# Kernel optimization log

Hardware: AMD Instinct MI355X
Metric: run time of the kernel (lower is better)

The kernel has to match this reference:

```python
import jax, jax.numpy as jnp
import numpy as np

N = 500_000   # total nodes across the batch of session graphs
B = 8192      # number of graphs
D = 128       # input_dim == output_dim (fc_out is None)
H = 128       # hidden_dim


def setup_inputs() -> dict:
    key = jax.random.key(0)
    ks = jax.random.split(key, 7)
    x_invar = jax.random.normal(ks[0], (N, D), jnp.float32)
    x_var = jax.random.normal(ks[1], (N, D), jnp.float32)
    s = 1.0 / np.sqrt(D)
    Wu = jax.random.normal(ks[2], (H, D), jnp.float32) * s
    bu = jnp.zeros((H,), jnp.float32)
    Wv = jax.random.normal(ks[3], (H, D), jnp.float32) * s
    We = jax.random.normal(ks[4], (1, H), jnp.float32) * (1.0 / np.sqrt(H))
    # sorted segment ids; guarantee every graph has >= 1 node
    seg_ids = jnp.sort(jnp.concatenate([
        jnp.arange(B, dtype=jnp.int32),
        jax.random.randint(ks[5], (N - B,), 0, B, dtype=jnp.int32),
    ]))
    # last node index of each graph = cumsum(counts) - 1
    counts = jax.ops.segment_sum(jnp.ones((N,), jnp.int32), seg_ids, num_segments=B)
    last_nodes = (jnp.cumsum(counts) - 1).astype(jnp.int32)
    return dict(x_invar=x_invar, x_var=x_var, Wu=Wu, bu=bu, Wv=Wv, We=We,
                seg_ids=seg_ids, last_nodes=last_nodes, num_graphs=B)


def _segment_softmax(e, seg, num_segments):
    # e: [M]; numerically stable per-segment softmax
    m = jax.ops.segment_max(e, seg, num_segments=num_segments)
    ex = jnp.exp(e - m[seg])
    den = jax.ops.segment_sum(ex, seg, num_segments=num_segments)
    return ex / den[seg]


def reference(x_invar, x_var, Wu, bu, Wv, We, seg_ids, last_nodes, num_graphs):
    # hybrid granularity, order=1: per-graph [invar; var] node rows.
    # Segment softmax/sum are permutation-invariant within a segment, so we
    # concatenate globally and double the segment ids.
    feats = jnp.concatenate([x_invar, x_var], axis=0)          # [2N, D]
    seg2 = jnp.concatenate([seg_ids, seg_ids], axis=0)         # [2N]
    feat_u = feats @ Wu.T + bu                                 # [2N, H]
    v_invar = (x_invar[last_nodes] @ Wv.T)[seg2]               # [2N, H]
    v_var = (x_var[last_nodes] @ Wv.T)[seg2]                   # [2N, H]
    e_invar = (jax.nn.sigmoid(feat_u + v_invar) @ We.T)[:, 0]  # [2N]
    e_var = (jax.nn.sigmoid(feat_u + v_var) @ We.T)[:, 0]      # [2N]
    a_invar = _segment_softmax(e_invar, seg2, num_graphs)[:, None]
    a_var = _segment_softmax(e_var, seg2, num_graphs)[:, None]
    rst_invar = jax.ops.segment_sum(feats * a_invar, seg2, num_segments=num_graphs)  # [B, D]
    rst_var = jax.ops.segment_sum(feats * a_var, seg2, num_segments=num_graphs)      # [B, D]
    return rst_invar[:, None, :], rst_var[:, None, :]          # [B, 1, D] each (order=1)
```

## Files before the change

kernel.cpp:

```cpp
#include <hip/hip_runtime.h>
#include <stdint.h>

typedef short short8 __attribute__((ext_vector_type(8)));
typedef float f32x4 __attribute__((ext_vector_type(4)));

#define D 128
#define LOG2E 1.44269504088896340736f

__device__ __forceinline__ unsigned short f2bf(float f) {
    union { float f; unsigned u; } v; v.f = f;
    unsigned u = v.u;
    unsigned r = (u + 0x7FFFu + ((u >> 16) & 1u)) >> 16;
    return (unsigned short)r;
}

__device__ __forceinline__ unsigned packbf(float x, float y) {
    unsigned ux = __float_as_uint(x) + 0x8000u;
    unsigned uy = __float_as_uint(y) + 0x8000u;
    return __builtin_amdgcn_perm(uy, ux, 0x07060302u);
}

template <int C>
__device__ __forceinline__ float dpp_add(float x) {
    int y = __builtin_amdgcn_update_dpp(0, __float_as_int(x), C, 0xF, 0xF, true);
    return x + __int_as_float(y);
}
__device__ __forceinline__ float red16(float x) {
    x = dpp_add<0xB1>(x);
    x = dpp_add<0x4E>(x);
    x = dpp_add<0x141>(x);
    x = dpp_add<0x140>(x);
    return x;
}

__global__ __launch_bounds__(256) void pack_wu(const float* __restrict__ Wu,
                                               short8* __restrict__ frag) {
    int tid = blockIdx.x * 256 + threadIdx.x;
    int nt = tid >> 8, kk = (tid >> 6) & 3, l = tid & 63;
    int col = nt * 16 + (l & 15);
    int kb  = kk * 32 + ((l >> 4) * 8);
    short8 o;
#pragma unroll
    for (int j = 0; j < 8; ++j) o[j] = (short)f2bf(Wu[col * D + kb + j] * LOG2E);
    frag[tid] = o;
}

__global__ __launch_bounds__(256) void gate_k(const float* __restrict__ xI,
                                              const float* __restrict__ xV,
                                              const float* __restrict__ Wv,
                                              const float* __restrict__ bu,
                                              const int* __restrict__ lastn,
                                              float* __restrict__ cIb,
                                              float* __restrict__ cVb, int B) {
    __shared__ __align__(16) float xs[4][2][D];
    int t = threadIdx.x, h = t & 127, st = t >> 7;
    float bias = bu[h];
    const float4* wv4 = (const float4*)(Wv + (size_t)h * D);
    const float* src = st ? xV : xI;
    float* dst = st ? cVb : cIb;
    int g0 = blockIdx.x * 16;
    for (int p = 0; p < 4; ++p) {
        int gb = g0 + p * 4;
#pragma unroll
        for (int j = 0; j < 4; ++j) {
            int gg = gb + j; if (gg >= B) gg = B - 1;
            xs[j][st][h] = src[(size_t)lastn[gg] * D + h];
        }
        __syncthreads();
        const float4* x0 = (const float4*)xs[0][st];
        const float4* x1 = (const float4*)xs[1][st];
        const float4* x2 = (const float4*)xs[2][st];
        const float4* x3 = (const float4*)xs[3][st];
        float a0 = 0.f, a1 = 0.f, a2 = 0.f, a3 = 0.f;
#pragma unroll
        for (int i = 0; i < 32; ++i) {
            float4 w = wv4[i], b;
            b = x0[i]; a0 += w.x*b.x + w.y*b.y + w.z*b.z + w.w*b.w;
            b = x1[i]; a1 += w.x*b.x + w.y*b.y + w.z*b.z + w.w*b.w;
            b = x2[i]; a2 += w.x*b.x + w.y*b.y + w.z*b.z + w.w*b.w;
            b = x3[i]; a3 += w.x*b.x + w.y*b.y + w.z*b.z + w.w*b.w;
        }
        if (gb + 0 < B) dst[(size_t)(gb+0)*D + h] = __builtin_amdgcn_exp2f(-(a0+bias)*LOG2E);
        if (gb + 1 < B) dst[(size_t)(gb+1)*D + h] = __builtin_amdgcn_exp2f(-(a1+bias)*LOG2E);
        if (gb + 2 < B) dst[(size_t)(gb+2)*D + h] = __builtin_amdgcn_exp2f(-(a2+bias)*LOG2E);
        if (gb + 3 < B) dst[(size_t)(gb+3)*D + h] = __builtin_amdgcn_exp2f(-(a3+bias)*LOG2E);
        __syncthreads();
    }
}

__global__ __launch_bounds__(256) void attn_main(
    const float* __restrict__ xI, const float* __restrict__ xV,
    const float* __restrict__ We, const int* __restrict__ lastn,
    const float* __restrict__ cIb, const float* __restrict__ cVb,
    const short8* __restrict__ fragG, float* __restrict__ out, int B) {
    __shared__ short8 bfrag[2048];
    __shared__ __align__(16) float wt[4][16][2];
    __shared__ float cmbA[2][4][D];
    __shared__ float cmbM[2][4], cmbL[2][4];

    int t = threadIdx.x, lane = t & 63, w = t >> 6;
    int g = blockIdx.x;

    {
        const uint4* srcf = (const uint4*)fragG;
        uint4* dst = (uint4*)bfrag;
#pragma unroll
        for (int i = 0; i < 8; ++i) dst[i * 256 + t] = srcf[i * 256 + t];
    }

    int s = (g == 0) ? 0 : (lastn[g - 1] + 1);
    int n = lastn[g] + 1 - s;

    float WeR[8], cIr[8], cVr[8];
#pragma unroll
    for (int nt = 0; nt < 8; ++nt) {
        int col = nt * 16 + (lane & 15);
        WeR[nt] = We[col] * LOG2E;
        cIr[nt] = cIb[(size_t)g * D + col];
        cVr[nt] = cVb[(size_t)g * D + col];
    }
    __syncthreads();

    float mI = -__builtin_inff(), mV = -__builtin_inff();
    float lIs = 0.f, lVs = 0.f;
    float aI0 = 0.f, aI1 = 0.f, aV0 = 0.f, aV1 = 0.f;

    int ch = (n + 15) >> 4;
    int total = 2 * ch;

    for (int c = w; c < total; c += 4) {
        int hf = (c >= ch) ? 1 : 0;
        const float* srcs = (hf ? xV : xI) + ((size_t)s << 7);
        int base = (c - hf * ch) << 4;

        int arow = base + (lane & 15);
        if (arow > n - 1) arow = n - 1;
        const float* rp = srcs + ((size_t)arow << 7) + ((lane >> 4) << 3);
        short8 af[4];
#pragma unroll
        for (int kk = 0; kk < 4; ++kk) {
            float4 f0 = *(const float4*)(rp + kk * 32);
            float4 f1 = *(const float4*)(rp + kk * 32 + 4);
            union { unsigned u[4]; short8 s8; } cv;
            cv.u[0] = packbf(f0.x, f0.y);
            cv.u[1] = packbf(f0.z, f0.w);
            cv.u[2] = packbf(f1.x, f1.y);
            cv.u[3] = packbf(f1.z, f1.w);
            af[kk] = cv.s8;
        }

        float pI[4] = {0.f, 0.f, 0.f, 0.f}, pV[4] = {0.f, 0.f, 0.f, 0.f};
#pragma unroll
        for (int nt = 0; nt < 8; ++nt) {
            f32x4 dacc = {0.f, 0.f, 0.f, 0.f};
#pragma unroll
            for (int kk = 0; kk < 4; ++kk)
                dacc = __builtin_amdgcn_mfma_f32_16x16x32_bf16(
                    af[kk], bfrag[nt * 256 + kk * 64 + lane], dacc, 0, 0, 0);
#pragma unroll
            for (int q = 0; q < 4; ++q) {
                float t2 = __builtin_amdgcn_exp2f(-dacc[q]);
                float dI = fmaf(t2, cIr[nt], 1.f);
                float dV = fmaf(t2, cVr[nt], 1.f);
                float rr = __builtin_amdgcn_rcpf(dI * dV);
                pI[q] = fmaf(WeR[nt], dV * rr, pI[q]);
                pV[q] = fmaf(WeR[nt], dI * rr, pV[q]);
            }
        }
#pragma unroll
        for (int q = 0; q < 4; ++q) { pI[q] = red16(pI[q]); pV[q] = red16(pV[q]); }
        if (base + 16 > n) {
#pragma unroll
            for (int q = 0; q < 4; ++q) {
                int r = ((lane >> 4) << 2) + q;
                if (base + r >= n) { pI[q] = -__builtin_inff(); pV[q] = -__builtin_inff(); }
            }
        }
        float cmI = fmaxf(fmaxf(pI[0], pI[1]), fmaxf(pI[2], pI[3]));
        float cmV = fmaxf(fmaxf(pV[0], pV[1]), fmaxf(pV[2], pV[3]));
        cmI = fmaxf(cmI, __shfl_xor(cmI, 16)); cmI = fmaxf(cmI, __shfl_xor(cmI, 32));
        cmV = fmaxf(cmV, __shfl_xor(cmV, 16)); cmV = fmaxf(cmV, __shfl_xor(cmV, 32));

        float mnI = fmaxf(mI, cmI), mnV = fmaxf(mV, cmV);
        float scI = __builtin_amdgcn_exp2f(mI - mnI);
        float scV = __builtin_amdgcn_exp2f(mV - mnV);
        lIs *= scI; lVs *= scV;
        aI0 *= scI; aI1 *= scI; aV0 *= scV; aV1 *= scV;

        float wIq[4], wVq[4];
#pragma unroll
        for (int q = 0; q < 4; ++q) {
            wIq[q] = __builtin_amdgcn_exp2f(pI[q] - mnI);
            wVq[q] = __builtin_amdgcn_exp2f(pV[q] - mnV);
        }
        float sIq = wIq[0] + wIq[1] + wIq[2] + wIq[3];
        float sVq = wVq[0] + wVq[1] + wVq[2] + wVq[3];
        sIq += __shfl_xor(sIq, 16); sIq += __shfl_xor(sIq, 32);
        sVq += __shfl_xor(sVq, 16); sVq += __shfl_xor(sVq, 32);
        lIs += sIq; lVs += sVq;

        if ((lane & 15) == 0) {
            int gq = lane >> 4;
            float4 w0 = {wIq[0], wVq[0], wIq[1], wVq[1]};
            float4 w1 = {wIq[2], wVq[2], wIq[3], wVq[3]};
            *(float4*)&wt[w][gq * 4 + 0][0] = w0;
            *(float4*)&wt[w][gq * 4 + 2][0] = w1;
        }
        asm volatile("" ::: "memory");

#pragma unroll
        for (int r = 0; r < 16; ++r) {
            int rr = base + r; if (rr > n - 1) rr = n - 1;
            const float* p = srcs + ((size_t)rr << 7);
            float f0 = p[lane], f1 = p[64 + lane];
            float wI = wt[w][r][0], wV = wt[w][r][1];
            aI0 = fmaf(wI, f0, aI0); aI1 = fmaf(wI, f1, aI1);
            aV0 = fmaf(wV, f0, aV0); aV1 = fmaf(wV, f1, aV1);
        }
        mI = mnI; mV = mnV;
    }

    cmbA[0][w][lane] = aI0; cmbA[0][w][lane + 64] = aI1;
    cmbA[1][w][lane] = aV0; cmbA[1][w][lane + 64] = aV1;
    if (lane == 0) {
        cmbM[0][w] = mI; cmbL[0][w] = lIs;
        cmbM[1][w] = mV; cmbL[1][w] = lVs;
    }
    __syncthreads();
    {
        int st = t >> 7, d = t & 127;
        float M = fmaxf(fmaxf(cmbM[st][0], cmbM[st][1]),
                        fmaxf(cmbM[st][2], cmbM[st][3]));
        float Ls = 0.f, A = 0.f;
#pragma unroll
        for (int ww = 0; ww < 4; ++ww) {
            float e = __builtin_amdgcn_exp2f(cmbM[st][ww] - M);
            Ls += cmbL[st][ww] * e;
            A  += cmbA[st][ww][d] * e;
        }
        out[(size_t)st * B * D + (size_t)g * D + d] = A * __builtin_amdgcn_rcpf(Ls);
    }
}

extern "C" void kernel_launch(void* const* d_in, const int* in_sizes, int n_in,
                              void* d_out, int out_size, void* d_ws, size_t ws_size,
                              hipStream_t stream) {
    const float* xI    = (const float*)d_in[0];
    const float* xV    = (const float*)d_in[1];
    const float* Wu    = (const float*)d_in[2];
    const float* bu    = (const float*)d_in[3];
    const float* Wv    = (const float*)d_in[4];
    const float* We    = (const float*)d_in[5];
    const int*   lastn = (const int*)d_in[7];
    const int B = in_sizes[7];

    float*  cIb   = (float*)d_ws;
    float*  cVb   = cIb + (size_t)B * D;
    short8* fragW = (short8*)(cVb + (size_t)B * D);

    pack_wu<<<8, 256, 0, stream>>>(Wu, fragW);
    gate_k<<<(B + 15) / 16, 256, 0, stream>>>(xI, xV, Wv, bu, lastn, cIb, cVb, B);
    attn_main<<<B, 256, 0, stream>>>(xI, xV, We, lastn, cIb, cVb, fragW,
                                     (float*)d_out, B);
}
```

Baseline: 220.8 us.

## Process four graphs per block to amortize weight-fragment LDS staging

Each attention block now handles four consecutive graphs in sequence instead of one, so the 32KB Wu fragment copy into shared memory and the We load are paid once per four graphs. The grid shrinks to B/4 blocks, which lowers parallelism and can hurt load balance across CUs when graph sizes vary. The weighted-sum loop also switches to float2 loads per lane with a matching column layout in the combine buffer. The grid size assumes B is divisible by 4, since any leftover graphs would be skipped.

```diff
diff --git a/kernel.cpp b/kernel.cpp
--- a/kernel.cpp
+++ b/kernel.cpp
@@ -6,6 +6,7 @@
 
 #define D 128
 #define LOG2E 1.44269504088896340736f
+#define GPB 4
 
 __device__ __forceinline__ unsigned short f2bf(float f) {
     union { float f; unsigned u; } v; v.f = f;
@@ -99,7 +100,6 @@
     __shared__ float cmbM[2][4], cmbL[2][4];
 
     int t = threadIdx.x, lane = t & 63, w = t >> 6;
-    int g = blockIdx.x;
 
     {
         const uint4* srcf = (const uint4*)fragG;
@@ -107,138 +107,152 @@
 #pragma unroll
         for (int i = 0; i < 8; ++i) dst[i * 256 + t] = srcf[i * 256 + t];
     }
-
-    int s = (g == 0) ? 0 : (lastn[g - 1] + 1);
-    int n = lastn[g] + 1 - s;
-
-    float WeR[8], cIr[8], cVr[8];
-#pragma unroll
-    for (int nt = 0; nt < 8; ++nt) {
-        int col = nt * 16 + (lane & 15);
-        WeR[nt] = We[col] * LOG2E;
-        cIr[nt] = cIb[(size_t)g * D + col];
-        cVr[nt] = cVb[(size_t)g * D + col];
-    }
+    float WeR[8];
+#pragma unroll
+    for (int nt = 0; nt < 8; ++nt) WeR[nt] = We[nt * 16 + (lane & 15)] * LOG2E;
     __syncthreads();
 
-    float mI = -__builtin_inff(), mV = -__builtin_inff();
-    float lIs = 0.f, lVs = 0.f;
-    float aI0 = 0.f, aI1 = 0.f, aV0 = 0.f, aV1 = 0.f;
-
-    int ch = (n + 15) >> 4;
-    int total = 2 * ch;
-
-    for (int c = w; c < total; c += 4) {
-        int hf = (c >= ch) ? 1 : 0;
-        const float* srcs = (hf ? xV : xI) + ((size_t)s << 7);
-        int base = (c - hf * ch) << 4;
-
-        int arow = base + (lane & 15);
-        if (arow > n - 1) arow = n - 1;
-        const float* rp = srcs + ((size_t)arow << 7) + ((lane >> 4) << 3);
-        short8 af[4];
-#pragma unroll
-        for (int kk = 0; kk < 4; ++kk) {
-            float4 f0 = *(const float4*)(rp + kk * 32);
-            float4 f1 = *(const float4*)(rp + kk * 32 + 4);
-            union { unsigned u[4]; short8 s8; } cv;
-            cv.u[0] = packbf(f0.x, f0.y);
-            cv.u[1] = packbf(f0.z, f0.w);
-            cv.u[2] = packbf(f1.x, f1.y);
-            cv.u[3] = packbf(f1.z, f1.w);
-            af[kk] = cv.s8;
-        }
-
-        float pI[4] = {0.f, 0.f, 0.f, 0.f}, pV[4] = {0.f, 0.f, 0.f, 0.f};
+    int g0 = blockIdx.x * GPB;
+    int sNext = (g0 == 0) ? 0 : (lastn[g0 - 1] + 1);
+
+    for (int gi = 0; gi < GPB; ++gi) {
+        int g = g0 + gi;
+        int s = sNext;
+        int e = lastn[g] + 1;
+        sNext = e;
+        int n = e - s;
+
+        float cIr[8], cVr[8];
 #pragma unroll
         for (int nt = 0; nt < 8; ++nt) {
-            f32x4 dacc = {0.f, 0.f, 0.f, 0.f};
-#pragma unroll
-            for (int kk = 0; kk < 4; ++kk)
-                dacc = __builtin_amdgcn_mfma_f32_16x16x32_bf16(
-                    af[kk], bfrag[nt * 256 + kk * 64 + lane], dacc, 0, 0, 0);
+            int col = nt * 16 + (lane & 15);
+            cIr[nt] = cIb[(size_t)g * D + col];
+            cVr[nt] = cVb[(size_t)g * D + col];
+        }
+
+        float mI = -__builtin_inff(), mV = -__builtin_inff();
+        float lIs = 0.f, lVs = 0.f;
+        float aI0 = 0.f, aI1 = 0.f, aV0 = 0.f, aV1 = 0.f;
+
+        int ch = (n + 15) >> 4;
+        int total = 2 * ch;
+
+        for (int c = w; c < total; c += 4) {
+            int hf = (c >= ch) ? 1 : 0;
+            const float* srcs = (hf ? xV : xI) + ((size_t)s << 7);
+            int base = (c - hf * ch) << 4;
+
+            int arow = base + (lane & 15);
+            if (arow > n - 1) arow = n - 1;
+            const float* rp = srcs + ((size_t)arow << 7) + ((lane >> 4) << 3);
+            short8 af[4];
+#pragma unroll
+            for (int kk = 0; kk < 4; ++kk) {
+                float4 f0 = *(const float4*)(rp + kk * 32);
+                float4 f1 = *(const float4*)(rp + kk * 32 + 4);
+                union { unsigned u[4]; short8 s8; } cv;
+                cv.u[0] = packbf(f0.x, f0.y);
+                cv.u[1] = packbf(f0.z, f0.w);
+                cv.u[2] = packbf(f1.x, f1.y);
+                cv.u[3] = packbf(f1.z, f1.w);
+                af[kk] = cv.s8;
+            }
+
+            float pI[4] = {0.f, 0.f, 0.f, 0.f}, pV[4] = {0.f, 0.f, 0.f, 0.f};
+#pragma unroll
+            for (int nt = 0; nt < 8; ++nt) {
+                f32x4 dacc = {0.f, 0.f, 0.f, 0.f};
+#pragma unroll
+                for (int kk = 0; kk < 4; ++kk)
+                    dacc = __builtin_amdgcn_mfma_f32_16x16x32_bf16(
+                        af[kk], bfrag[nt * 256 + kk * 64 + lane], dacc, 0, 0, 0);
+#pragma unroll
+                for (int q = 0; q < 4; ++q) {
+                    float t2 = __builtin_amdgcn_exp2f(-dacc[q]);
+                    float dI = fmaf(t2, cIr[nt], 1.f);
+                    float dV = fmaf(t2, cVr[nt], 1.f);
+                    float rr = __builtin_amdgcn_rcpf(dI * dV);
+                    pI[q] = fmaf(WeR[nt], dV * rr, pI[q]);
+                    pV[q] = fmaf(WeR[nt], dI * rr, pV[q]);
+                }
+            }
+#pragma unroll
+            for (int q = 0; q < 4; ++q) { pI[q] = red16(pI[q]); pV[q] = red16(pV[q]); }
+            if (base + 16 > n) {
+#pragma unroll
+                for (int q = 0; q < 4; ++q) {
+                    int r = ((lane >> 4) << 2) + q;
+                    if (base + r >= n) { pI[q] = -__builtin_inff(); pV[q] = -__builtin_inff(); }
+                }
+            }
+            float cmI = fmaxf(fmaxf(pI[0], pI[1]), fmaxf(pI[2], pI[3]));
+            float cmV = fmaxf(fmaxf(pV[0], pV[1]), fmaxf(pV[2], pV[3]));
+            cmI = fmaxf(cmI, __shfl_xor(cmI, 16)); cmI = fmaxf(cmI, __shfl_xor(cmI, 32));
+            cmV = fmaxf(cmV, __shfl_xor(cmV, 16)); cmV = fmaxf(cmV, __shfl_xor(cmV, 32));
+
+            float mnI = fmaxf(mI, cmI), mnV = fmaxf(mV, cmV);
+            float scI = __builtin_amdgcn_exp2f(mI - mnI);
+            float scV = __builtin_amdgcn_exp2f(mV - mnV);
+            lIs *= scI; lVs *= scV;
+            aI0 *= scI; aI1 *= scI; aV0 *= scV; aV1 *= scV;
+
+            float wIq[4], wVq[4];
 #pragma unroll
             for (int q = 0; q < 4; ++q) {
-                float t2 = __builtin_amdgcn_exp2f(-dacc[q]);
-                float dI = fmaf(t2, cIr[nt], 1.f);
-                float dV = fmaf(t2, cVr[nt], 1.f);
-                float rr = __builtin_amdgcn_rcpf(dI * dV);
-                pI[q] = fmaf(WeR[nt], dV * rr, pI[q]);
-                pV[q] = fmaf(WeR[nt], dI * rr, pV[q]);
-            }
-        }
-#pragma unroll
-        for (int q = 0; q < 4; ++q) { pI[q] = red16(pI[q]); pV[q] = red16(pV[q]); }
-        if (base + 16 > n) {
-#pragma unroll
-            for (int q = 0; q < 4; ++q) {
-                int r = ((lane >> 4) << 2) + q;
-                if (base + r >= n) { pI[q] = -__builtin_inff(); pV[q] = -__builtin_inff(); }
-            }
-        }
-        float cmI = fmaxf(fmaxf(pI[0], pI[1]), fmaxf(pI[2], pI[3]));
-        float cmV = fmaxf(fmaxf(pV[0], pV[1]), fmaxf(pV[2], pV[3]));
-        cmI = fmaxf(cmI, __shfl_xor(cmI, 16)); cmI = fmaxf(cmI, __shfl_xor(cmI, 32));
-        cmV = fmaxf(cmV, __shfl_xor(cmV, 16)); cmV = fmaxf(cmV, __shfl_xor(cmV, 32));
-
-        float mnI = fmaxf(mI, cmI), mnV = fmaxf(mV, cmV);
-        float scI = __builtin_amdgcn_exp2f(mI - mnI);
-        float scV = __builtin_amdgcn_exp2f(mV - mnV);
-        lIs *= scI; lVs *= scV;
-        aI0 *= scI; aI1 *= scI; aV0 *= scV; aV1 *= scV;
-
-        float wIq[4], wVq[4];
-#pragma unroll
-        for (int q = 0; q < 4; ++q) {
-            wIq[q] = __builtin_amdgcn_exp2f(pI[q] - mnI);
-            wVq[q] = __builtin_amdgcn_exp2f(pV[q] - mnV);
-        }
-        float sIq = wIq[0] + wIq[1] + wIq[2] + wIq[3];
-        float sVq = wVq[0] + wVq[1] + wVq[2] + wVq[3];
-        sIq += __shfl_xor(sIq, 16); sIq += __shfl_xor(sIq, 32);
-        sVq += __shfl_xor(sVq, 16); sVq += __shfl_xor(sVq, 32);
-        lIs += sIq; lVs += sVq;
-
-        if ((lane & 15) == 0) {
-            int gq = lane >> 4;
-            float4 w0 = {wIq[0], wVq[0], wIq[1], wVq[1]};
-            float4 w1 = {wIq[2], wVq[2], wIq[3], wVq[3]};
-            *(float4*)&wt[w][gq * 4 + 0][0] = w0;
-            *(float4*)&wt[w][gq * 4 + 2][0] = w1;
-        }
-        asm volatile("" ::: "memory");
-
-#pragma unroll
-        for (int r = 0; r < 16; ++r) {
-            int rr = base + r; if (rr > n - 1) rr = n - 1;
-            const float* p = srcs + ((size_t)rr << 7);
-            float f0 = p[lane], f1 = p[64 + lane];
-            float wI = wt[w][r][0], wV = wt[w][r][1];
-            aI0 = fmaf(wI, f0, aI0); aI1 = fmaf(wI, f1, aI1);
-            aV0 = fmaf(wV, f0, aV0); aV1 = fmaf(wV, f1, aV1);
-        }
-        mI = mnI; mV = mnV;
-    }
-
-    cmbA[0][w][lane] = aI0; cmbA[0][w][lane + 64] = aI1;
-    cmbA[1][w][lane] = aV0; cmbA[1][w][lane + 64] = aV1;
-    if (lane == 0) {
-        cmbM[0][w] = mI; cmbL[0][w] = lIs;
-        cmbM[1][w] = mV; cmbL[1][w] = lVs;
-    }
-    __syncthreads();
-    {
-        int st = t >> 7, d = t & 127;
-        float M = fmaxf(fmaxf(cmbM[st][0], cmbM[st][1]),
-                        fmaxf(cmbM[st][2], cmbM[st][3]));
-        float Ls = 0.f, A = 0.f;
-#pragma unroll
-        for (int ww = 0; ww < 4; ++ww) {
-            float e = __builtin_amdgcn_exp2f(cmbM[st][ww] - M);
-            Ls += cmbL[st][ww] * e;
-            A  += cmbA[st][ww][d] * e;
-        }
-        out[(size_t)st * B * D + (size_t)g * D + d] = A * __builtin_amdgcn_rcpf(Ls);
+                wIq[q] = __builtin_amdgcn_exp2f(pI[q] - mnI);
+                wVq[q] = __builtin_amdgcn_exp2f(pV[q] - mnV);
+            }
+            float sIq = wIq[0] + wIq[1] + wIq[2] + wIq[3];
+            float sVq = wVq[0] + wVq[1] + wVq[2] + wVq[3];
+            sIq += __shfl_xor(sIq, 16); sIq += __shfl_xor(sIq, 32);
+            sVq += __shfl_xor(sVq, 16); sVq += __shfl_xor(sVq, 32);
+            lIs += sIq; lVs += sVq;
+
+            if ((lane & 15) == 0) {
+                int gq = lane >> 4;
+                float4 w0 = {wIq[0], wVq[0], wIq[1], wVq[1]};
+                float4 w1 = {wIq[2], wVq[2], wIq[3], wVq[3]};
+                *(float4*)&wt[w][gq * 4 + 0][0] = w0;
+                *(float4*)&wt[w][gq * 4 + 2][0] = w1;
+            }
+            asm volatile("" ::: "memory");
+
+            const float2* s2 = (const float2*)srcs;
+#pragma unroll
+            for (int r = 0; r < 16; ++r) {
+                int rr = base + r; if (rr > n - 1) rr = n - 1;
+                float2 f = s2[((size_t)rr << 6) + lane];
+                float2 wv = *(const float2*)&wt[w][r][0];
+                aI0 = fmaf(wv.x, f.x, aI0); aI1 = fmaf(wv.x, f.y, aI1);
+                aV0 = fmaf(wv.y, f.x, aV0); aV1 = fmaf(wv.y, f.y, aV1);
+            }
+            mI = mnI; mV = mnV;
+        }
+
+        __syncthreads();
+        {
+            float2 vI = {aI0, aI1}, vV = {aV0, aV1};
+            *(float2*)&cmbA[0][w][lane * 2] = vI;
+            *(float2*)&cmbA[1][w][lane * 2] = vV;
+        }
+        if (lane == 0) {
+            cmbM[0][w] = mI; cmbL[0][w] = lIs;
+            cmbM[1][w] = mV; cmbL[1][w] = lVs;
+        }
+        __syncthreads();
+        {
+            int st = t >> 7, d = t & 127;
+            float M = fmaxf(fmaxf(cmbM[st][0], cmbM[st][1]),
+                            fmaxf(cmbM[st][2], cmbM[st][3]));
+            float Ls = 0.f, A = 0.f;
+#pragma unroll
+            for (int ww = 0; ww < 4; ++ww) {
+                float e2 = __builtin_amdgcn_exp2f(cmbM[st][ww] - M);
+                Ls += cmbL[st][ww] * e2;
+                A  += cmbA[st][ww][d] * e2;
+            }
+            out[(size_t)st * B * D + (size_t)g * D + d] = A * __builtin_amdgcn_rcpf(Ls);
+        }
     }
 }
 
@@ -260,6 +274,6 @@
 
     pack_wu<<<8, 256, 0, stream>>>(Wu, fragW);
     gate_k<<<(B + 15) / 16, 256, 0, stream>>>(xI, xV, Wv, bu, lastn, cIb, cVb, B);
-    attn_main<<<B, 256, 0, stream>>>(xI, xV, We, lastn, cIb, cVb, fragW,
-                                     (float*)d_out, B);
-}
+    attn_main<<<B / GPB, 256, 0, stream>>>(xI, xV, We, lastn, cIb, cVb, fragW,
+                                           (float*)d_out, B);
+}
```

Result: no change. 220.4 us (-0.2%).
